# Kernel tuning notes

Measured on AMD Instinct MI355X. Metric: run time of the kernel, lower is better.

Reference implementation:

```python
import jax, jax.numpy as jnp
import numpy as np

EPS = 1e-08

def setup_inputs() -> dict:
    key = jax.random.key(0)
    ks = jax.random.split(key, 5)
    B, T, D, L = 8, 4096, 1024, 24
    data = jax.random.normal(ks[0], (B, T, D), dtype=jnp.float32)
    W_enc = jax.random.normal(ks[1], (L, D), dtype=jnp.float32) * (1.0 / np.sqrt(D))
    b_enc = jax.random.normal(ks[2], (L,), dtype=jnp.float32) * 0.01
    W_dec = jax.random.normal(ks[3], (D, L), dtype=jnp.float32) * (1.0 / np.sqrt(L))
    b_dec = jax.random.normal(ks[4], (D,), dtype=jnp.float32) * 0.01
    ecs = jnp.array([0.1], dtype=jnp.float32)  # error_correction_strength
    ep = jnp.array([1.0], dtype=jnp.float32)   # energy_preservation
    return {"data": data, "W_enc": W_enc, "b_enc": b_enc,
            "W_dec": W_dec, "b_dec": b_dec,
            "error_correction_strength": ecs, "energy_preservation": ep}

def _l2(x):
    return jnp.linalg.norm(x, axis=-1, keepdims=True)

def reference(data, W_enc, b_enc, W_dec, b_dec, error_correction_strength, energy_preservation):
    ecs = error_correction_strength[0]
    ep = energy_preservation[0]
    # --- encode_to_lattice ---
    in_e = _l2(data)                                   # [B,T,1]
    proj = jnp.einsum('btd,ld->btl', data, W_enc) + b_enc
    lattice_points = jnp.round(proj / ecs) * ecs       # quantize to lattice grid
    out_e = _l2(lattice_points)
    lattice = lattice_points * (in_e / (out_e + EPS)) * ep
    # --- decode_from_lattice ---
    in_e2 = _l2(lattice)
    corrected = jnp.where(jnp.abs(lattice) > ecs, lattice, 0.0)
    res = jnp.einsum('btl,dl->btd', corrected, W_dec) + b_dec
    out_e2 = _l2(res)
    return res * (in_e2 / (out_e2 + EPS)) * ep
```

## Files before the change

kernel.cpp:

```cpp
#include <hip/hip_runtime.h>
#include <math.h>

#define EPS 1e-8f

__global__ void prep_all(const float* __restrict__ W_enc,
                         const float* __restrict__ Wd, const float* __restrict__ bd,
                         float* __restrict__ wt, float* __restrict__ G,
                         float* __restrict__ h, float* __restrict__ bb) {
    int b = blockIdx.x;
    int lane = threadIdx.x;
    if (b < 384) {
        int i = b * 64 + lane;
        int k = i / 24, l = i - k * 24;
        wt[i] = W_enc[l * 1024 + k];
        return;
    }
    b -= 384;
    float s = 0.f;
    if (b < 576) {
        int l = b / 24, m = b - (b / 24) * 24;
        for (int d = lane; d < 1024; d += 64) s = fmaf(Wd[d * 24 + l], Wd[d * 24 + m], s);
    } else if (b < 600) {
        int l = b - 576;
        for (int d = lane; d < 1024; d += 64) s = fmaf(Wd[d * 24 + l], bd[d], s);
    } else {
        for (int d = lane; d < 1024; d += 64) s = fmaf(bd[d], bd[d], s);
    }
    for (int off = 32; off; off >>= 1) s += __shfl_down(s, off);
    if (lane == 0) {
        if (b < 576) G[b] = s;
        else if (b < 600) h[b - 576] = s;
        else *bb = s;
    }
}


constexpr int LD_TILE = 33;
constexpr int TILE_F  = 64 * LD_TILE;
constexpr int SMEM_F  = 4 * TILE_F;

__global__ __launch_bounds__(256, 4)
void leech_main(const float* __restrict__ data,
                const float* __restrict__ b_enc,
                const float* __restrict__ Wd,
                const float* __restrict__ b_dec,
                const float* __restrict__ ecs_p,
                const float* __restrict__ ep_p,
                const float* __restrict__ wt,
                const float* __restrict__ G,
                const float* __restrict__ h,
                const float* __restrict__ bbp,
                float* __restrict__ out)
{
    __shared__ float smem[SMEM_F];
    const int tid = threadIdx.x;
    const int w = tid >> 6;
    const int r = tid & 63;
    const int rowbase = blockIdx.x * 64;

    float* tile = smem + w * TILE_F;

    const int lrow = r >> 3;
    const int lk   = (r & 7) * 4;

    float proj[24];
#pragma unroll
    for (int l = 0; l < 24; ++l) proj[l] = 0.f;
    float ssq = 0.f;

    const int kw = __builtin_amdgcn_readfirstlane((tid >> 6) * 256);

    float4 buf[8];
#pragma unroll
    for (int it = 0; it < 8; ++it)
        buf[it] = *reinterpret_cast<const float4*>(
            data + (size_t)(rowbase + it * 8 + lrow) * 1024 + kw + lk);

    for (int sc = 0; sc < 8; ++sc) {
#pragma unroll
        for (int it = 0; it < 8; ++it) {
            float* t = tile + (it * 8 + lrow) * LD_TILE + lk;
            t[0] = buf[it].x; t[1] = buf[it].y; t[2] = buf[it].z; t[3] = buf[it].w;
        }
        if (sc < 7) {
            const int k0n = kw + (sc + 1) * 32;
#pragma unroll
            for (int it = 0; it < 8; ++it)
                buf[it] = *reinterpret_cast<const float4*>(
                    data + (size_t)(rowbase + it * 8 + lrow) * 1024 + k0n + lk);
        }
        const float* xrow = tile + r * LD_TILE;
        const int kofs = __builtin_amdgcn_readfirstlane(kw + sc * 32);
#pragma unroll 8
        for (int kk = 0; kk < 32; ++kk) {
            const float x = xrow[kk];
            ssq = fmaf(x, x, ssq);
            const float* wp = wt + (size_t)(kofs + kk) * 24;
#pragma unroll
            for (int l = 0; l < 24; ++l)
                proj[l] = fmaf(wp[l], x, proj[l]);
        }
    }

#pragma unroll
    for (int l = 0; l < 24; ++l)
        smem[w * TILE_F + l * 64 + r] = proj[l];
    smem[w * TILE_F + 24 * 64 + r] = ssq;
    __syncthreads();

    float p[24];
#pragma unroll
    for (int l = 0; l < 24; ++l)
        p[l] = (smem[0 * TILE_F + l * 64 + r] + smem[1 * TILE_F + l * 64 + r]) +
               (smem[2 * TILE_F + l * 64 + r] + smem[3 * TILE_F + l * 64 + r]);
    const float ss = (smem[0 * TILE_F + 24 * 64 + r] + smem[1 * TILE_F + 24 * 64 + r]) +
                     (smem[2 * TILE_F + 24 * 64 + r] + smem[3 * TILE_F + 24 * 64 + r]);
    __syncthreads();

    const float ecs = ecs_p[0];
    const float ep  = ep_p[0];
    const float in_e = sqrtf(ss);

    float lp[24]; float oe = 0.f;
#pragma unroll
    for (int l = 0; l < 24; ++l) {
        const float pp = p[l] + b_enc[l];
        const float q = rintf(pp / ecs) * ecs;
        lp[l] = q;
        oe = fmaf(q, q, oe);
    }
    const float s1 = in_e / (sqrtf(oe) + EPS) * ep;

    float c[24]; float ie = 0.f;
#pragma unroll
    for (int l = 0; l < 24; ++l) {
        const float lat = lp[l] * s1;
        ie = fmaf(lat, lat, ie);
        c[l] = (fabsf(lat) > ecs) ? lat : 0.f;
    }
    const float in_e2 = sqrtf(ie);

    float qacc = bbp[0];
#pragma unroll
    for (int l = 0; l < 24; ++l) {
        float s = 2.f * h[l];
#pragma unroll
        for (int m = 0; m < 24; ++m)
            s = fmaf(G[l * 24 + m], c[m], s);
        qacc = fmaf(s, c[l], qacc);
    }
    const float out_e2 = sqrtf(fmaxf(qacc, 0.f));
    const float s2 = in_e2 / (out_e2 + EPS) * ep;

    for (int sc = 0; sc < 8; ++sc) {
        const int d0 = __builtin_amdgcn_readfirstlane(kw + sc * 32);
        float* trow = tile + r * LD_TILE;
#pragma unroll 4
        for (int dd = 0; dd < 32; ++dd) {
            const int d = d0 + dd;
            const float* wr = Wd + d * 24;
            float acc = b_dec[d];
#pragma unroll
            for (int l = 0; l < 24; ++l)
                acc = fmaf(wr[l], c[l], acc);
            trow[dd] = acc * s2;
        }
#pragma unroll
        for (int it = 0; it < 8; ++it) {
            const float* t = tile + (it * 8 + lrow) * LD_TILE + lk;
            float4 v; v.x = t[0]; v.y = t[1]; v.z = t[2]; v.w = t[3];
            *reinterpret_cast<float4*>(
                out + (size_t)(rowbase + it * 8 + lrow) * 1024 + d0 + lk) = v;
        }
    }
}


extern "C" void kernel_launch(void* const* d_in, const int* in_sizes, int n_in,
                              void* d_out, int out_size, void* d_ws, size_t ws_size,
                              hipStream_t stream) {
    const float* data  = (const float*)d_in[0];
    const float* W_enc = (const float*)d_in[1];
    const float* b_enc = (const float*)d_in[2];
    const float* W_dec = (const float*)d_in[3];
    const float* b_dec = (const float*)d_in[4];
    const float* ecs   = (const float*)d_in[5];
    const float* ep    = (const float*)d_in[6];
    float* out = (float*)d_out;

    float* ws = (float*)d_ws;
    float* wt = ws;
    float* G  = ws + 24576;
    float* h  = ws + 25152;
    float* bb = ws + 25176;

    const int rows = in_sizes[0] / 1024;

    hipLaunchKernelGGL(prep_all, dim3(985), dim3(64), 0, stream,
                       W_enc, W_dec, b_dec, wt, G, h, bb);
    hipLaunchKernelGGL(leech_main, dim3(rows / 64), dim3(256), 0, stream,
                       data, b_enc, W_dec, b_dec, ecs, ep, wt, G, h, bb, out);
}
```

Baseline: 323.7 us.

## Split row-block K dimension across eight wavefronts instead of four

Each 64-row block now uses 512 threads (8 waves), with each wave covering 128 columns of D instead of 256, staged in 16-column chunks through a smaller shared-memory tile. The goal is more memory-level parallelism and more waves in flight per block to hide load latency on this bandwidth-bound kernel. In exchange, the cross-wave reduction of the 24 projections reads twice as many partial sums, and the float4 loads and stores now cover narrower 64-byte row segments.

```diff
diff --git a/kernel.cpp b/kernel.cpp
--- a/kernel.cpp
+++ b/kernel.cpp
@@ -35,11 +35,11 @@
 }
 
 
-constexpr int LD_TILE = 33;
-constexpr int TILE_F  = 64 * LD_TILE;
-constexpr int SMEM_F  = 4 * TILE_F;
-
-__global__ __launch_bounds__(256, 4)
+constexpr int LD_TILE  = 21;
+constexpr int REGION_F = 1600;
+constexpr int SMEM_F   = 8 * REGION_F;
+
+__global__ __launch_bounds__(512, 2)
 void leech_main(const float* __restrict__ data,
                 const float* __restrict__ b_enc,
                 const float* __restrict__ Wd,
@@ -58,41 +58,41 @@
     const int r = tid & 63;
     const int rowbase = blockIdx.x * 64;
 
-    float* tile = smem + w * TILE_F;
-
-    const int lrow = r >> 3;
-    const int lk   = (r & 7) * 4;
+    float* tile = smem + w * REGION_F;
+
+    const int lrow = r & 15;
+    const int lk   = (r >> 4) * 4;
+
+    const int kw = __builtin_amdgcn_readfirstlane((tid >> 6) * 128);
 
     float proj[24];
 #pragma unroll
     for (int l = 0; l < 24; ++l) proj[l] = 0.f;
     float ssq = 0.f;
 
-    const int kw = __builtin_amdgcn_readfirstlane((tid >> 6) * 256);
-
-    float4 buf[8];
-#pragma unroll
-    for (int it = 0; it < 8; ++it)
+    float4 buf[4];
+#pragma unroll
+    for (int it = 0; it < 4; ++it)
         buf[it] = *reinterpret_cast<const float4*>(
-            data + (size_t)(rowbase + it * 8 + lrow) * 1024 + kw + lk);
+            data + (size_t)(rowbase + it * 16 + lrow) * 1024 + kw + lk);
 
     for (int sc = 0; sc < 8; ++sc) {
 #pragma unroll
-        for (int it = 0; it < 8; ++it) {
-            float* t = tile + (it * 8 + lrow) * LD_TILE + lk;
+        for (int it = 0; it < 4; ++it) {
+            float* t = tile + (it * 16 + lrow) * LD_TILE + lk;
             t[0] = buf[it].x; t[1] = buf[it].y; t[2] = buf[it].z; t[3] = buf[it].w;
         }
         if (sc < 7) {
-            const int k0n = kw + (sc + 1) * 32;
-#pragma unroll
-            for (int it = 0; it < 8; ++it)
+            const int k0n = kw + (sc + 1) * 16;
+#pragma unroll
+            for (int it = 0; it < 4; ++it)
                 buf[it] = *reinterpret_cast<const float4*>(
-                    data + (size_t)(rowbase + it * 8 + lrow) * 1024 + k0n + lk);
+                    data + (size_t)(rowbase + it * 16 + lrow) * 1024 + k0n + lk);
         }
         const float* xrow = tile + r * LD_TILE;
-        const int kofs = __builtin_amdgcn_readfirstlane(kw + sc * 32);
+        const int kofs = __builtin_amdgcn_readfirstlane(kw + sc * 16);
 #pragma unroll 8
-        for (int kk = 0; kk < 32; ++kk) {
+        for (int kk = 0; kk < 16; ++kk) {
             const float x = xrow[kk];
             ssq = fmaf(x, x, ssq);
             const float* wp = wt + (size_t)(kofs + kk) * 24;
@@ -104,17 +104,27 @@
 
 #pragma unroll
     for (int l = 0; l < 24; ++l)
-        smem[w * TILE_F + l * 64 + r] = proj[l];
-    smem[w * TILE_F + 24 * 64 + r] = ssq;
+        smem[w * REGION_F + l * 64 + r] = proj[l];
+    smem[w * REGION_F + 24 * 64 + r] = ssq;
     __syncthreads();
 
     float p[24];
 #pragma unroll
-    for (int l = 0; l < 24; ++l)
-        p[l] = (smem[0 * TILE_F + l * 64 + r] + smem[1 * TILE_F + l * 64 + r]) +
-               (smem[2 * TILE_F + l * 64 + r] + smem[3 * TILE_F + l * 64 + r]);
-    const float ss = (smem[0 * TILE_F + 24 * 64 + r] + smem[1 * TILE_F + 24 * 64 + r]) +
-                     (smem[2 * TILE_F + 24 * 64 + r] + smem[3 * TILE_F + 24 * 64 + r]);
+    for (int l = 0; l < 24; ++l) {
+        float a0 = smem[0 * REGION_F + l * 64 + r] + smem[1 * REGION_F + l * 64 + r];
+        float a1 = smem[2 * REGION_F + l * 64 + r] + smem[3 * REGION_F + l * 64 + r];
+        float a2 = smem[4 * REGION_F + l * 64 + r] + smem[5 * REGION_F + l * 64 + r];
+        float a3 = smem[6 * REGION_F + l * 64 + r] + smem[7 * REGION_F + l * 64 + r];
+        p[l] = (a0 + a1) + (a2 + a3);
+    }
+    float ss;
+    {
+        float a0 = smem[0 * REGION_F + 24 * 64 + r] + smem[1 * REGION_F + 24 * 64 + r];
+        float a1 = smem[2 * REGION_F + 24 * 64 + r] + smem[3 * REGION_F + 24 * 64 + r];
+        float a2 = smem[4 * REGION_F + 24 * 64 + r] + smem[5 * REGION_F + 24 * 64 + r];
+        float a3 = smem[6 * REGION_F + 24 * 64 + r] + smem[7 * REGION_F + 24 * 64 + r];
+        ss = (a0 + a1) + (a2 + a3);
+    }
     __syncthreads();
 
     const float ecs = ecs_p[0];
@@ -153,10 +163,10 @@
     const float s2 = in_e2 / (out_e2 + EPS) * ep;
 
     for (int sc = 0; sc < 8; ++sc) {
-        const int d0 = __builtin_amdgcn_readfirstlane(kw + sc * 32);
+        const int d0 = __builtin_amdgcn_readfirstlane(kw + sc * 16);
         float* trow = tile + r * LD_TILE;
 #pragma unroll 4
-        for (int dd = 0; dd < 32; ++dd) {
+        for (int dd = 0; dd < 16; ++dd) {
             const int d = d0 + dd;
             const float* wr = Wd + d * 24;
             float acc = b_dec[d];
@@ -166,11 +176,11 @@
             trow[dd] = acc * s2;
         }
 #pragma unroll
-        for (int it = 0; it < 8; ++it) {
-            const float* t = tile + (it * 8 + lrow) * LD_TILE + lk;
+        for (int it = 0; it < 4; ++it) {
+            const float* t = tile + (it * 16 + lrow) * LD_TILE + lk;
             float4 v; v.x = t[0]; v.y = t[1]; v.z = t[2]; v.w = t[3];
             *reinterpret_cast<float4*>(
-                out + (size_t)(rowbase + it * 8 + lrow) * 1024 + d0 + lk) = v;
+                out + (size_t)(rowbase + it * 16 + lrow) * 1024 + d0 + lk) = v;
         }
     }
 }
@@ -198,6 +208,6 @@
 
     hipLaunchKernelGGL(prep_all, dim3(985), dim3(64), 0, stream,
                        W_enc, W_dec, b_dec, wt, G, h, bb);
-    hipLaunchKernelGGL(leech_main, dim3(rows / 64), dim3(256), 0, stream,
+    hipLaunchKernelGGL(leech_main, dim3(rows / 64), dim3(512), 0, stream,
                        data, b_enc, W_dec, b_dec, ecs, ep, wt, G, h, bb, out);
 }
```

After: 326.0 us. No clear change (+0.7%).
